# Optimization experiments

Measured on AMD Instinct MI355X. Metric: run time of the kernel, lower is better.

## Reference

```python
import jax, jax.numpy as jnp
import numpy as np

CHUNK = 2048  # row tile size; keeps the [CHUNK, M] tile ~268 MB


def setup_inputs() -> dict:
    key = jax.random.key(0)
    k1, k2, k3 = jax.random.split(key, 3)
    N, M, D = 32768, 32768, 32
    ls = jax.random.uniform(k1, (1,), dtype=jnp.float32, minval=0.1, maxval=1.0)
    x = jax.random.normal(k2, (N, D), dtype=jnp.float32)
    y = jax.random.normal(k3, (M, D), dtype=jnp.float32)
    return {"ls": ls, "x": x, "y": y}


def reference(ls, x, y):
    # out[i] = sum_j exp(-ls * ||x_i - y_j||^2), computed in row tiles
    # (never materializes the full N x M matrix, like KeOps Genred).
    N, D = x.shape
    y_sq = jnp.sum(y * y, axis=1)  # [M]

    def row_chunk(xc):
        # xc: [CHUNK, D]
        x_sq = jnp.sum(xc * xc, axis=1)  # [CHUNK]
        sq = x_sq[:, None] + y_sq[None, :] - 2.0 * (xc @ y.T)  # [CHUNK, M]
        return jnp.sum(jnp.exp(-ls[0] * sq), axis=1)  # [CHUNK]

    x_tiles = x.reshape(N // CHUNK, CHUNK, D)
    out = jax.lax.map(row_chunk, x_tiles)  # [N//CHUNK, CHUNK]
    return out.reshape(N, 1)
```

## Files before the change

### kernel.cpp

```cpp
#include <hip/hip_runtime.h>
#include <math.h>

#define DIM 32
#define BLK 256
#define JSPLIT 16
#define ITPB 8
#define RI   2

typedef _Float16 half8 __attribute__((ext_vector_type(8)));
typedef float    f32x4 __attribute__((ext_vector_type(4)));


__global__ __launch_bounds__(BLK) void rbf_prep(
    const float* __restrict__ lsp, const float* __restrict__ x,
    const float* __restrict__ y, int n, int m,
    double* __restrict__ acc, double* __restrict__ scale,
    float* __restrict__ bf,
    half8* __restrict__ xfh, half8* __restrict__ xfl,
    half8* __restrict__ yfh, half8* __restrict__ yfl)
{
    int i = blockIdx.x * BLK + threadIdx.x;
    const double c2 = -(double)lsp[0] * 1.4426950408889634074;
    const float mf = (float)(-2.0 * c2);
    if (i < n) {
        const float* xp = x + (size_t)i * DIM;
        double xs = 0.0;
        #pragma unroll
        for (int d = 0; d < DIM; ++d) { double v = (double)xp[d]; xs = fma(v, v, xs); }
        acc[i] = 0.0;
        scale[i] = exp2(c2 * xs);
        const int it = i >> 4, r15 = i & 15;
        #pragma unroll
        for (int q = 0; q < 4; ++q) {
            half8 hh, hl;
            #pragma unroll
            for (int d = 0; d < 8; ++d) {
                float v = xp[q * 8 + d] * mf;
                _Float16 h = (_Float16)v;
                hh[d] = h;
                hl[d] = (_Float16)((v - (float)h) * 4096.0f);
            }
            xfh[it * 64 + q * 16 + r15] = hh;
            xfl[it * 64 + q * 16 + r15] = hl;
        }
    }
    if (i < m) {
        const float* yp = y + (size_t)i * DIM;
        double ys = 0.0;
        #pragma unroll
        for (int d = 0; d < DIM; ++d) { double v = (double)yp[d]; ys = fma(v, v, ys); }
        bf[i] = (float)(c2 * ys);
        const int it = i >> 4, r15 = i & 15;
        #pragma unroll
        for (int q = 0; q < 4; ++q) {
            half8 hh, hl;
            #pragma unroll
            for (int d = 0; d < 8; ++d) {
                float v = yp[q * 8 + d];
                _Float16 h = (_Float16)v;
                hh[d] = h;
                hl[d] = (_Float16)((v - (float)h) * 4096.0f);
            }
            yfh[it * 64 + q * 16 + r15] = hh;
            yfl[it * 64 + q * 16 + r15] = hl;
        }
    }
}

__global__ __launch_bounds__(BLK, 4) void rbf_main(
    const half8* __restrict__ xfh, const half8* __restrict__ xfl,
    const half8* __restrict__ yfh, const half8* __restrict__ yfl,
    const float* __restrict__ bf, double* __restrict__ acc, int chunk_j)
{
    const int lane = threadIdx.x & 63;
    const int wave = threadIdx.x >> 6;
    const int itbase = blockIdx.x * ITPB + wave * RI;

    half8 ah[RI], al[RI];
    #pragma unroll
    for (int r = 0; r < RI; ++r) {
        ah[r] = xfh[(itbase + r) * 64 + lane];
        al[r] = xfl[(itbase + r) * 64 + lane];
    }

    const int jt0 = (blockIdx.y * chunk_j) >> 4;
    const int njt = chunk_j >> 4;
    const int c15 = lane & 15;

    double accd[RI][4];
    #pragma unroll
    for (int r = 0; r < RI; ++r)
        #pragma unroll
        for (int e = 0; e < 4; ++e) accd[r][e] = 0.0;

    half8 bh = yfh[jt0 * 64 + lane];
    half8 bl = yfl[jt0 * 64 + lane];
    float bfv = bf[jt0 * 16 + c15];

    for (int g = 0; g < njt / 8; ++g) {
        float accf[RI][4];
        #pragma unroll
        for (int r = 0; r < RI; ++r)
            #pragma unroll
            for (int e = 0; e < 4; ++e) accf[r][e] = 0.0f;

        #pragma unroll
        for (int tt = 0; tt < 8; ++tt) {
            const int jt = jt0 + g * 8 + tt;
            int jn = jt + 1; if (jn >= jt0 + njt) jn = jt0;
            half8 bh_n = yfh[jn * 64 + lane];
            half8 bl_n = yfl[jn * 64 + lane];
            float bf_n = bf[jn * 16 + c15];

            #pragma unroll
            for (int r = 0; r < RI; ++r) {
                f32x4 cm = {bfv, bfv, bfv, bfv};
                cm = __builtin_amdgcn_mfma_f32_16x16x32_f16(ah[r], bh, cm, 0, 0, 0);
                f32x4 cl = {0.0f, 0.0f, 0.0f, 0.0f};
                cl = __builtin_amdgcn_mfma_f32_16x16x32_f16(ah[r], bl, cl, 0, 0, 0);
                cl = __builtin_amdgcn_mfma_f32_16x16x32_f16(al[r], bh, cl, 0, 0, 0);
                #pragma unroll
                for (int e = 0; e < 4; ++e) {
                    float f = __builtin_fmaf(cl[e], 0x1p-12f, cm[e]);
                    accf[r][e] += __builtin_amdgcn_exp2f(f);
                }
            }
            bh = bh_n; bl = bl_n; bfv = bf_n;
        }
        #pragma unroll
        for (int r = 0; r < RI; ++r)
            #pragma unroll
            for (int e = 0; e < 4; ++e) accd[r][e] += (double)accf[r][e];
    }

    #pragma unroll
    for (int r = 0; r < RI; ++r) {
        #pragma unroll
        for (int e = 0; e < 4; ++e) {
            double v = accd[r][e];
            v += __shfl_xor(v, 1, 64);
            v += __shfl_xor(v, 2, 64);
            v += __shfl_xor(v, 4, 64);
            v += __shfl_xor(v, 8, 64);
            if (c15 == 0) {
                int row = (itbase + r) * 16 + (lane >> 4) * 4 + e;
                atomicAdd(&acc[row], v);
            }
        }
    }
}

__global__ __launch_bounds__(BLK) void rbf_finish(
    const double* __restrict__ acc, const double* __restrict__ scale,
    float* __restrict__ out, int n)
{
    int i = blockIdx.x * BLK + threadIdx.x;
    if (i < n) out[i] = (float)(acc[i] * scale[i]);
}

extern "C" void kernel_launch(void* const* d_in, const int* in_sizes, int n_in,
                              void* d_out, int out_size, void* d_ws, size_t ws_size,
                              hipStream_t stream)
{
    const float* ls = (const float*)d_in[0];
    const float* x  = (const float*)d_in[1];
    const float* y  = (const float*)d_in[2];
    const int n = in_sizes[1] / DIM;
    const int m = in_sizes[2] / DIM;
    float* out = (float*)d_out;

    char* ws = (char*)d_ws;
    double* acc   = (double*)ws;
    double* scale = acc + n;
    float*  bf    = (float*)(scale + n);
    half8*  xfh   = (half8*)(bf + m);
    half8*  xfl   = xfh + (size_t)n * 4;
    half8*  yfh   = xfl + (size_t)n * 4;
    half8*  yfl   = yfh + (size_t)m * 4;

    const int nm = (n > m) ? n : m;
    rbf_prep<<<(nm + BLK - 1) / BLK, BLK, 0, stream>>>(
        ls, x, y, n, m, acc, scale, bf, xfh, xfl, yfh, yfl);

    const int chunk = m / JSPLIT;
    dim3 grid(n / (16 * ITPB), JSPLIT);
    rbf_main<<<grid, BLK, 0, stream>>>(xfh, xfl, yfh, yfl, bf, acc, chunk);

    rbf_finish<<<(n + BLK - 1) / BLK, BLK, 0, stream>>>(acc, scale, out, n);
}
```

Baseline: 318.0 us.

## Interleave hi/lo fp16 operands, use packed f32x2 epilogue, lengthen float accumulation group

Stores the hi and lo fp16 halves of each x/y fragment next to each other in one 32-byte struct, so each lane gets both with one contiguous load. The fp32-to-fp64 flush now happens every 16 tiles instead of every 8. The fma and accumulate epilogue is rewritten with 2-wide float vectors so the compiler can emit packed FMA/add instructions. The longer fp32 accumulation window may slightly reduce accuracy.

```diff
diff --git a/kernel.cpp b/kernel.cpp
--- a/kernel.cpp
+++ b/kernel.cpp
@@ -6,18 +6,20 @@
 #define JSPLIT 16
 #define ITPB 8
 #define RI   2
+#define GTT  16
 
 typedef _Float16 half8 __attribute__((ext_vector_type(8)));
 typedef float    f32x4 __attribute__((ext_vector_type(4)));
+typedef float    f32x2 __attribute__((ext_vector_type(2)));
+
+struct hl16 { half8 h; half8 l; };
 
 
 __global__ __launch_bounds__(BLK) void rbf_prep(
     const float* __restrict__ lsp, const float* __restrict__ x,
     const float* __restrict__ y, int n, int m,
     double* __restrict__ acc, double* __restrict__ scale,
-    float* __restrict__ bf,
-    half8* __restrict__ xfh, half8* __restrict__ xfl,
-    half8* __restrict__ yfh, half8* __restrict__ yfl)
+    float* __restrict__ bf, hl16* __restrict__ xhl, hl16* __restrict__ yhl)
 {
     int i = blockIdx.x * BLK + threadIdx.x;
     const double c2 = -(double)lsp[0] * 1.4426950408889634074;
@@ -40,8 +42,8 @@
                 hh[d] = h;
                 hl[d] = (_Float16)((v - (float)h) * 4096.0f);
             }
-            xfh[it * 64 + q * 16 + r15] = hh;
-            xfl[it * 64 + q * 16 + r15] = hl;
+            xhl[it * 64 + q * 16 + r15].h = hh;
+            xhl[it * 64 + q * 16 + r15].l = hl;
         }
     }
     if (i < m) {
@@ -61,31 +63,33 @@
                 hh[d] = h;
                 hl[d] = (_Float16)((v - (float)h) * 4096.0f);
             }
-            yfh[it * 64 + q * 16 + r15] = hh;
-            yfl[it * 64 + q * 16 + r15] = hl;
+            yhl[it * 64 + q * 16 + r15].h = hh;
+            yhl[it * 64 + q * 16 + r15].l = hl;
         }
     }
 }
 
 __global__ __launch_bounds__(BLK, 4) void rbf_main(
-    const half8* __restrict__ xfh, const half8* __restrict__ xfl,
-    const half8* __restrict__ yfh, const half8* __restrict__ yfl,
+    const hl16* __restrict__ xhl, const hl16* __restrict__ yhl,
     const float* __restrict__ bf, double* __restrict__ acc, int chunk_j)
 {
     const int lane = threadIdx.x & 63;
     const int wave = threadIdx.x >> 6;
     const int itbase = blockIdx.x * ITPB + wave * RI;
+    const int c15 = lane & 15;
 
     half8 ah[RI], al[RI];
     #pragma unroll
     for (int r = 0; r < RI; ++r) {
-        ah[r] = xfh[(itbase + r) * 64 + lane];
-        al[r] = xfl[(itbase + r) * 64 + lane];
+        ah[r] = xhl[(itbase + r) * 64 + lane].h;
+        al[r] = xhl[(itbase + r) * 64 + lane].l;
     }
 
     const int jt0 = (blockIdx.y * chunk_j) >> 4;
     const int njt = chunk_j >> 4;
-    const int c15 = lane & 15;
+
+    const f32x4 zq = {0.0f, 0.0f, 0.0f, 0.0f};
+    const float k12 = 0x1p-12f;
 
     double accd[RI][4];
     #pragma unroll
@@ -93,44 +97,51 @@
         #pragma unroll
         for (int e = 0; e < 4; ++e) accd[r][e] = 0.0;
 
-    half8 bh = yfh[jt0 * 64 + lane];
-    half8 bl = yfl[jt0 * 64 + lane];
+    half8 bh = yhl[(size_t)jt0 * 64 + lane].h;
+    half8 bl = yhl[(size_t)jt0 * 64 + lane].l;
     float bfv = bf[jt0 * 16 + c15];
 
-    for (int g = 0; g < njt / 8; ++g) {
-        float accf[RI][4];
+    for (int g = 0; g < njt / GTT; ++g) {
+        f32x2 accf[RI][2];
         #pragma unroll
-        for (int r = 0; r < RI; ++r)
-            #pragma unroll
-            for (int e = 0; e < 4; ++e) accf[r][e] = 0.0f;
+        for (int r = 0; r < RI; ++r) {
+            accf[r][0] = (f32x2){0.0f, 0.0f};
+            accf[r][1] = (f32x2){0.0f, 0.0f};
+        }
 
         #pragma unroll
-        for (int tt = 0; tt < 8; ++tt) {
-            const int jt = jt0 + g * 8 + tt;
+        for (int tt = 0; tt < GTT; ++tt) {
+            const int jt = jt0 + g * GTT + tt;
             int jn = jt + 1; if (jn >= jt0 + njt) jn = jt0;
-            half8 bh_n = yfh[jn * 64 + lane];
-            half8 bl_n = yfl[jn * 64 + lane];
-            float bf_n = bf[jn * 16 + c15];
+            const hl16* __restrict__ yt = yhl + (size_t)jn * 64;
+            half8 bh_n = yt[lane].h;
+            half8 bl_n = yt[lane].l;
+            float bf_n = (bf + jn * 16)[c15];
 
+            const f32x4 cbf = {bfv, bfv, bfv, bfv};
             #pragma unroll
             for (int r = 0; r < RI; ++r) {
-                f32x4 cm = {bfv, bfv, bfv, bfv};
-                cm = __builtin_amdgcn_mfma_f32_16x16x32_f16(ah[r], bh, cm, 0, 0, 0);
-                f32x4 cl = {0.0f, 0.0f, 0.0f, 0.0f};
-                cl = __builtin_amdgcn_mfma_f32_16x16x32_f16(ah[r], bl, cl, 0, 0, 0);
+                f32x4 cm = __builtin_amdgcn_mfma_f32_16x16x32_f16(ah[r], bh, cbf, 0, 0, 0);
+                f32x4 cl = __builtin_amdgcn_mfma_f32_16x16x32_f16(ah[r], bl, zq, 0, 0, 0);
                 cl = __builtin_amdgcn_mfma_f32_16x16x32_f16(al[r], bh, cl, 0, 0, 0);
-                #pragma unroll
-                for (int e = 0; e < 4; ++e) {
-                    float f = __builtin_fmaf(cl[e], 0x1p-12f, cm[e]);
-                    accf[r][e] += __builtin_amdgcn_exp2f(f);
-                }
+                f32x2 f0 = {cm[0], cm[1]}, f1 = {cm[2], cm[3]};
+                f32x2 l0 = {cl[0], cl[1]}, l1 = {cl[2], cl[3]};
+                f0 = l0 * k12 + f0;
+                f1 = l1 * k12 + f1;
+                f32x2 e0 = {__builtin_amdgcn_exp2f(f0.x), __builtin_amdgcn_exp2f(f0.y)};
+                f32x2 e1 = {__builtin_amdgcn_exp2f(f1.x), __builtin_amdgcn_exp2f(f1.y)};
+                accf[r][0] += e0;
+                accf[r][1] += e1;
             }
             bh = bh_n; bl = bl_n; bfv = bf_n;
         }
         #pragma unroll
-        for (int r = 0; r < RI; ++r)
-            #pragma unroll
-            for (int e = 0; e < 4; ++e) accd[r][e] += (double)accf[r][e];
+        for (int r = 0; r < RI; ++r) {
+            accd[r][0] += (double)accf[r][0].x;
+            accd[r][1] += (double)accf[r][0].y;
+            accd[r][2] += (double)accf[r][1].x;
+            accd[r][3] += (double)accf[r][1].y;
+        }
     }
 
     #pragma unroll
@@ -173,18 +184,16 @@
     double* acc   = (double*)ws;
     double* scale = acc + n;
     float*  bf    = (float*)(scale + n);
-    half8*  xfh   = (half8*)(bf + m);
-    half8*  xfl   = xfh + (size_t)n * 4;
-    half8*  yfh   = xfl + (size_t)n * 4;
-    half8*  yfl   = yfh + (size_t)m * 4;
+    hl16*   xhl   = (hl16*)(bf + m);
+    hl16*   yhl   = xhl + (size_t)(n / 16) * 64;
 
     const int nm = (n > m) ? n : m;
     rbf_prep<<<(nm + BLK - 1) / BLK, BLK, 0, stream>>>(
-        ls, x, y, n, m, acc, scale, bf, xfh, xfl, yfh, yfl);
+        ls, x, y, n, m, acc, scale, bf, xhl, yhl);
 
     const int chunk = m / JSPLIT;
     dim3 grid(n / (16 * ITPB), JSPLIT);
-    rbf_main<<<grid, BLK, 0, stream>>>(xfh, xfl, yfh, yfl, bf, acc, chunk);
+    rbf_main<<<grid, BLK, 0, stream>>>(xhl, yhl, bf, acc, chunk);
 
     rbf_finish<<<(n + BLK - 1) / BLK, BLK, 0, stream>>>(acc, scale, out, n);
 }
```

New measurement: 322.3 us. About the same (+1.3%).
